# Kernel tuning notes

Measured on AMD Instinct MI355X. Metric: run time of the kernel, lower is better.

## Reference

```python
import jax, jax.numpy as jnp
import numpy as np

L_SEQ = 4096   # sequence length L
E = 1024       # embedding_size
NL = 8         # num_layers
H = 4 * E      # channel-mix hidden
V = 4          # LocalHilDim
LOGP_FACTOR = 0.5


def setup_inputs() -> dict:
    key = jax.random.key(0)
    ks = jax.random.split(key, 20)
    n = lambda k, shp, s=0.02: jax.random.normal(k, shp, jnp.float32) * s
    u = lambda k, shp: jax.random.uniform(k, shp, dtype=jnp.float32)
    return {
        "s": jax.random.randint(ks[0], (L_SEQ,), 0, V),
        "embed": n(ks[1], (V, E), 1.0),
        # TimeMixing params, stacked over layers
        "tm_first": jnp.log(jnp.float32(0.3)) + n(ks[2], (NL, E), 0.5),
        "tm_decay": -5.0 + 8.0 * u(ks[3], (NL, E)),
        "tm_mk": u(ks[4], (NL, E)),
        "tm_mv": u(ks[5], (NL, E)),
        "tm_mr": u(ks[6], (NL, E)),
        "tm_Wk": n(ks[7], (NL, E, E)),
        "tm_Wv": n(ks[8], (NL, E, E)),
        "tm_Wr": n(ks[9], (NL, E, E)),
        "tm_Wo": n(ks[10], (NL, E, E)),
        # ChannelMixing params
        "cm_mk": u(ks[11], (NL, E)),
        "cm_mr": u(ks[12], (NL, E)),
        "cm_Wk": n(ks[13], (NL, E, H)),
        "cm_Wr": n(ks[14], (NL, E, E)),
        "cm_Wv": n(ks[15], (NL, H, E)),
        # Neck / Head
        "neck_W": n(ks[16], (E, E)),
        "neck_b": jnp.zeros((E,), jnp.float32),
        "head_W": n(ks[17], (E, V)),
    }


def _wkv(k, v, time_first, time_decay):
    """Max-stabilized RWKV WKV recurrence over time. k,v: [L,E]."""
    z = jnp.zeros_like(k[0])
    init = (z, z, jnp.full_like(k[0], -jnp.inf))  # aa, bb, pp

    def step(carry, kv):
        aa, bb, pp = carry
        kk, vv = kv
        ww = time_first + kk
        p = jnp.maximum(pp, ww)
        e1 = jnp.exp(pp - p)
        e2 = jnp.exp(ww - p)
        out = (e1 * aa + e2 * vv) / (e1 * bb + e2)
        ww = pp - jnp.exp(time_decay)
        p = jnp.maximum(ww, kk)
        e1 = jnp.exp(ww - p)
        e2 = jnp.exp(kk - p)
        return (e1 * aa + e2 * vv, e1 * bb + e2, p), out

    _, out = jax.lax.scan(step, init, (k, v))
    return out


def _shift(x):
    # prepend zero-state row, drop last (token-shift with zero initial state)
    return jnp.concatenate([jnp.zeros_like(x[:1]), x[:-1]], axis=0)


def _block(x, p):
    # --- TimeMixing ---
    sx = _shift(x)
    kx = x * p["tm_mk"] + sx * (1 - p["tm_mk"])
    vx = x * p["tm_mv"] + sx * (1 - p["tm_mv"])
    rx = x * p["tm_mr"] + sx * (1 - p["tm_mr"])
    r = jax.nn.sigmoid(rx @ p["tm_Wr"])
    k = kx @ p["tm_Wk"]
    v = vx @ p["tm_Wv"]
    wkv = _wkv(k, v, p["tm_first"], p["tm_decay"])
    x = x + (r * wkv) @ p["tm_Wo"]
    # --- ChannelMixing ---
    sx = _shift(x)
    xk = x * p["cm_mk"] + sx * (1 - p["cm_mk"])
    xr = x * p["cm_mr"] + sx * (1 - p["cm_mr"])
    r = jax.nn.sigmoid(xr @ p["cm_Wr"])
    kk = jnp.square(jax.nn.relu(xk @ p["cm_Wk"]))  # [L, 4E]
    x = x + r * (kk @ p["cm_Wv"])
    return x


def reference(s, embed, tm_first, tm_decay, tm_mk, tm_mv, tm_mr,
              tm_Wk, tm_Wv, tm_Wr, tm_Wo, cm_mk, cm_mr, cm_Wk, cm_Wr, cm_Wv,
              neck_W, neck_b, head_W):
    tok = jnp.pad(s[:-1], (1, 0))
    x = embed[tok]                          # [L, E]
    layer_params = {
        "tm_first": tm_first, "tm_decay": tm_decay,
        "tm_mk": tm_mk, "tm_mv": tm_mv, "tm_mr": tm_mr,
        "tm_Wk": tm_Wk, "tm_Wv": tm_Wv, "tm_Wr": tm_Wr, "tm_Wo": tm_Wo,
        "cm_mk": cm_mk, "cm_mr": cm_mr,
        "cm_Wk": cm_Wk, "cm_Wr": cm_Wr, "cm_Wv": cm_Wv,
    }

    def body(x, p):
        return _block(x, p), None

    x, _ = jax.lax.scan(body, x, layer_params)  # scan over NL layers
    x = jax.nn.gelu(x @ neck_W + neck_b)
    logits = x @ head_W                         # [L, V]
    logp = jax.nn.log_softmax(logits) * LOGP_FACTOR
    # log-amplitude of configuration s (Q is None -> no mask, no penalty)
    return jnp.take_along_axis(logp, s[:, None], axis=-1).sum(axis=-2).squeeze(-1)
```

## Files before the change

### kernel.cpp

```cpp
#include <hip/hip_runtime.h>
#include <stdint.h>

#define L_SEQ 4096
#define EDIM  1024
#define HDIM  4096
#define NLAY  8
#define WKV_C 128
#define WKV_T 32
#define SCAN_LANES 16
#define SCAN_CPT   (WKV_C / SCAN_LANES)

typedef unsigned short u16;
typedef __attribute__((ext_vector_type(8))) short short8;
typedef __attribute__((ext_vector_type(4))) float f32x4;
typedef __attribute__((ext_vector_type(4))) unsigned short us4;
typedef __attribute__((ext_vector_type(8))) unsigned short us8;

static __device__ __forceinline__ u16 f2b(float f) {
  union { float f; uint32_t u; } a; a.f = f;
  uint32_t u = a.u;
  return (u16)((u + 0x7FFFu + ((u >> 16) & 1u)) >> 16);
}
static __device__ __forceinline__ float b2f(u16 b) {
  union { uint32_t u; float f; } a; a.u = ((uint32_t)b) << 16;
  return a.f;
}
static __device__ __forceinline__ float sigm(float v) {
  return 1.f / (1.f + __expf(-v));
}
static __device__ __forceinline__ float4 ld_bf4(const u16* __restrict__ p, size_t i) {
  us4 v = *reinterpret_cast<const us4*>(&p[i]);
  return make_float4(b2f(v.x), b2f(v.y), b2f(v.z), b2f(v.w));
}

static __device__ __forceinline__ void gld_lds16(const void* g, void* l) {
  __builtin_amdgcn_global_load_lds(
      (const __attribute__((address_space(1))) void*)g,
      (__attribute__((address_space(3))) void*)l, 16, 0, 0);
}


__global__ void k_f0(const int* __restrict__ s, const float* __restrict__ embed,
                     const float* __restrict__ mk, const float* __restrict__ mv,
                     const float* __restrict__ mr, u16* __restrict__ xA,
                     u16* __restrict__ kx, u16* __restrict__ vx, u16* __restrict__ rx) {
  int i = (blockIdx.x * blockDim.x + threadIdx.x) * 4;
  int t = i >> 10, e = i & 1023;
  int tok = (t == 0) ? 0 : s[t - 1];
  float4 xc = *reinterpret_cast<const float4*>(&embed[tok * EDIM + e]);
  float4 xs = make_float4(0.f, 0.f, 0.f, 0.f);
  if (t > 0) {
    int tokp = (t == 1) ? 0 : s[t - 2];
    xs = *reinterpret_cast<const float4*>(&embed[tokp * EDIM + e]);
  }
  us4 ox; ox.x = f2b(xc.x); ox.y = f2b(xc.y); ox.z = f2b(xc.z); ox.w = f2b(xc.w);
  *reinterpret_cast<us4*>(&xA[i]) = ox;
  float4 m; us4 o;
  m = *reinterpret_cast<const float4*>(&mk[e]);
  o.x = f2b(xc.x * m.x + xs.x * (1.f - m.x)); o.y = f2b(xc.y * m.y + xs.y * (1.f - m.y));
  o.z = f2b(xc.z * m.z + xs.z * (1.f - m.z)); o.w = f2b(xc.w * m.w + xs.w * (1.f - m.w));
  *reinterpret_cast<us4*>(&kx[i]) = o;
  m = *reinterpret_cast<const float4*>(&mv[e]);
  o.x = f2b(xc.x * m.x + xs.x * (1.f - m.x)); o.y = f2b(xc.y * m.y + xs.y * (1.f - m.y));
  o.z = f2b(xc.z * m.z + xs.z * (1.f - m.z)); o.w = f2b(xc.w * m.w + xs.w * (1.f - m.w));
  *reinterpret_cast<us4*>(&vx[i]) = o;
  m = *reinterpret_cast<const float4*>(&mr[e]);
  o.x = f2b(xc.x * m.x + xs.x * (1.f - m.x)); o.y = f2b(xc.y * m.y + xs.y * (1.f - m.y));
  o.z = f2b(xc.z * m.z + xs.z * (1.f - m.z)); o.w = f2b(xc.w * m.w + xs.w * (1.f - m.w));
  *reinterpret_cast<us4*>(&rx[i]) = o;
}

static __device__ __forceinline__ float4 cm_finish(const u16* __restrict__ xB,
                                                   const u16* __restrict__ PR,
                                                   const u16* __restrict__ PB, int i) {
  const size_t LE = (size_t)L_SEQ * EDIM;
  float4 xm = ld_bf4(xB, i);
  float4 r0 = ld_bf4(PR, i), r1 = ld_bf4(PR, i + LE);
  float4 v0 = ld_bf4(PB, i), v1 = ld_bf4(PB, i + LE);
  float4 v2 = ld_bf4(PB, i + 2 * LE), v3 = ld_bf4(PB, i + 3 * LE);
  xm.x += sigm(r0.x + r1.x) * (v0.x + v1.x + v2.x + v3.x);
  xm.y += sigm(r0.y + r1.y) * (v0.y + v1.y + v2.y + v3.y);
  xm.z += sigm(r0.z + r1.z) * (v0.z + v1.z + v2.z + v3.z);
  xm.w += sigm(r0.w + r1.w) * (v0.w + v1.w + v2.w + v3.w);
  return xm;
}

__global__ void k_f1(const u16* __restrict__ xB, const u16* __restrict__ PR,
                     const u16* __restrict__ PB,
                     const float* __restrict__ mk, const float* __restrict__ mv,
                     const float* __restrict__ mr, u16* __restrict__ xA,
                     u16* __restrict__ kx, u16* __restrict__ vx, u16* __restrict__ rx) {
  int i = (blockIdx.x * blockDim.x + threadIdx.x) * 4;
  int e = i & 1023;
  float4 xc = cm_finish(xB, PR, PB, i);
  float4 xs = make_float4(0.f, 0.f, 0.f, 0.f);
  if (i >= EDIM) xs = cm_finish(xB, PR, PB, i - EDIM);
  us4 ox; ox.x = f2b(xc.x); ox.y = f2b(xc.y); ox.z = f2b(xc.z); ox.w = f2b(xc.w);
  *reinterpret_cast<us4*>(&xA[i]) = ox;
  float4 m; us4 o;
  m = *reinterpret_cast<const float4*>(&mk[e]);
  o.x = f2b(xc.x * m.x + xs.x * (1.f - m.x)); o.y = f2b(xc.y * m.y + xs.y * (1.f - m.y));
  o.z = f2b(xc.z * m.z + xs.z * (1.f - m.z)); o.w = f2b(xc.w * m.w + xs.w * (1.f - m.w));
  *reinterpret_cast<us4*>(&kx[i]) = o;
  m = *reinterpret_cast<const float4*>(&mv[e]);
  o.x = f2b(xc.x * m.x + xs.x * (1.f - m.x)); o.y = f2b(xc.y * m.y + xs.y * (1.f - m.y));
  o.z = f2b(xc.z * m.z + xs.z * (1.f - m.z)); o.w = f2b(xc.w * m.w + xs.w * (1.f - m.w));
  *reinterpret_cast<us4*>(&vx[i]) = o;
  m = *reinterpret_cast<const float4*>(&mr[e]);
  o.x = f2b(xc.x * m.x + xs.x * (1.f - m.x)); o.y = f2b(xc.y * m.y + xs.y * (1.f - m.y));
  o.z = f2b(xc.z * m.z + xs.z * (1.f - m.z)); o.w = f2b(xc.w * m.w + xs.w * (1.f - m.w));
  *reinterpret_cast<us4*>(&rx[i]) = o;
}

static __device__ __forceinline__ float4 tm_finish(const u16* __restrict__ xA,
                                                   const u16* __restrict__ PA, int i) {
  const size_t LE = (size_t)L_SEQ * EDIM;
  float4 xm = ld_bf4(xA, i);
  float4 a = ld_bf4(PA, i), b = ld_bf4(PA, i + LE);
  xm.x += a.x + b.x; xm.y += a.y + b.y; xm.z += a.z + b.z; xm.w += a.w + b.w;
  return xm;
}

__global__ void k_f2(const u16* __restrict__ xA, const u16* __restrict__ PA,
                     const float* __restrict__ mk, const float* __restrict__ mr,
                     u16* __restrict__ xB, u16* __restrict__ kx, u16* __restrict__ rx) {
  int i = (blockIdx.x * blockDim.x + threadIdx.x) * 4;
  int e = i & 1023;
  float4 xc = tm_finish(xA, PA, i);
  float4 xs = make_float4(0.f, 0.f, 0.f, 0.f);
  if (i >= EDIM) xs = tm_finish(xA, PA, i - EDIM);
  us4 ox; ox.x = f2b(xc.x); ox.y = f2b(xc.y); ox.z = f2b(xc.z); ox.w = f2b(xc.w);
  *reinterpret_cast<us4*>(&xB[i]) = ox;
  float4 m; us4 o;
  m = *reinterpret_cast<const float4*>(&mk[e]);
  o.x = f2b(xc.x * m.x + xs.x * (1.f - m.x)); o.y = f2b(xc.y * m.y + xs.y * (1.f - m.y));
  o.z = f2b(xc.z * m.z + xs.z * (1.f - m.z)); o.w = f2b(xc.w * m.w + xs.w * (1.f - m.w));
  *reinterpret_cast<us4*>(&kx[i]) = o;
  m = *reinterpret_cast<const float4*>(&mr[e]);
  o.x = f2b(xc.x * m.x + xs.x * (1.f - m.x)); o.y = f2b(xc.y * m.y + xs.y * (1.f - m.y));
  o.z = f2b(xc.z * m.z + xs.z * (1.f - m.z)); o.w = f2b(xc.w * m.w + xs.w * (1.f - m.w));
  *reinterpret_cast<us4*>(&rx[i]) = o;
}

__global__ void k_f3(const u16* __restrict__ xB, const u16* __restrict__ PR,
                     const u16* __restrict__ PB, u16* __restrict__ hb) {
  int i = (blockIdx.x * blockDim.x + threadIdx.x) * 4;
  float4 xc = cm_finish(xB, PR, PB, i);
  us4 o;
  o.x = f2b(xc.x); o.y = f2b(xc.y); o.z = f2b(xc.z); o.w = f2b(xc.w);
  *reinterpret_cast<us4*>(&hb[i]) = o;
}

static __device__ __forceinline__ float gelu1(float v) {
  float c = 0.7978845608028654f * (v + 0.044715f * v * v * v);
  return 0.5f * v * (1.f + tanhf(c));
}

static __device__ __forceinline__
void tconv2(const float* __restrict__ s, u16* __restrict__ d, int K, int N,
            int n0, int k0) {
  __shared__ float tile[64][65];
  int tid = threadIdx.x;
  int tx = tid & 15, ty = tid >> 4;
#pragma unroll
  for (int i = 0; i < 4; ++i) {
    int kr = ty + i * 16;
    float4 v = *reinterpret_cast<const float4*>(&s[(size_t)(k0 + kr) * N + n0 + tx * 4]);
    tile[kr][tx * 4 + 0] = v.x; tile[kr][tx * 4 + 1] = v.y;
    tile[kr][tx * 4 + 2] = v.z; tile[kr][tx * 4 + 3] = v.w;
  }
  __syncthreads();
  int tx8 = tid & 7, ny = tid >> 3;
#pragma unroll
  for (int h = 0; h < 2; ++h) {
    int n = ny + h * 32;
    us8 o;
#pragma unroll
    for (int c = 0; c < 8; ++c) o[c] = f2b(tile[tx8 * 8 + c][n]);
    *reinterpret_cast<us8*>(&d[(size_t)(n0 + n) * K + k0 + tx8 * 8]) = o;
  }
}

__global__ __launch_bounds__(256)
void k_tconv(const float* __restrict__ src, u16* __restrict__ dst, int K, int N) {
  tconv2(src + (size_t)blockIdx.z * K * N, dst + (size_t)blockIdx.z * K * N,
         K, N, blockIdx.x * 64, blockIdx.y * 64);
}

#define TC_EE  (41 * 256)
#define TC_EH  8192
__global__ __launch_bounds__(256)
void k_tconv_all(const float* __restrict__ Wk, const float* __restrict__ Wv,
                 const float* __restrict__ Wr, const float* __restrict__ Wo,
                 const float* __restrict__ cWr, const float* __restrict__ nW,
                 const float* __restrict__ cWk, const float* __restrict__ cWv,
                 u16* __restrict__ oWk, u16* __restrict__ oWv, u16* __restrict__ oWr,
                 u16* __restrict__ oWo, u16* __restrict__ ocWr, u16* __restrict__ onW,
                 u16* __restrict__ ocWk, u16* __restrict__ ocWv) {
  const size_t EE = (size_t)EDIM * EDIM, EH = (size_t)EDIM * HDIM;
  int bid = blockIdx.x;
  if (bid < TC_EE) {
    int z = bid >> 8, rem = bid & 255;
    const float* src; u16* dst;
    if (z < 8)       { src = Wk  + (size_t)z * EE;        dst = oWk  + (size_t)z * EE; }
    else if (z < 16) { src = Wv  + (size_t)(z - 8) * EE;  dst = oWv  + (size_t)(z - 8) * EE; }
    else if (z < 24) { src = Wr  + (size_t)(z - 16) * EE; dst = oWr  + (size_t)(z - 16) * EE; }
    else if (z < 32) { src = Wo  + (size_t)(z - 24) * EE; dst = oWo  + (size_t)(z - 24) * EE; }
    else if (z < 40) { src = cWr + (size_t)(z - 32) * EE; dst = ocWr + (size_t)(z - 32) * EE; }
    else             { src = nW;                          dst = onW; }
    tconv2(src, dst, EDIM, EDIM, (rem & 15) * 64, (rem >> 4) * 64);
  } else if (bid < TC_EE + TC_EH) {
    int b = bid - TC_EE;
    int z = b >> 10, rem = b & 1023;
    tconv2(cWk + (size_t)z * EH, ocWk + (size_t)z * EH, EDIM, HDIM,
           (rem & 63) * 64, (rem >> 6) * 64);
  } else {
    int b = bid - TC_EE - TC_EH;
    int z = b >> 10, rem = b & 1023;
    tconv2(cWv + (size_t)z * EH, ocWv + (size_t)z * EH, HDIM, EDIM,
           (rem & 15) * 64, (rem >> 4) * 64);
  }
}

template <int EPI>
__device__ __forceinline__
void g256_body(const u16* __restrict__ A, const u16* __restrict__ Bt,
               void* __restrict__ Cv, int N, int ldk, int klen,
               int bm, int bn) {
  extern __shared__ __align__(16) u16 lds[];
  const int tid = threadIdx.x, lane = tid & 63, w = tid >> 6;
  const int wr = w >> 2, wc = w & 3;
  const int l16 = lane & 15, lhi = lane >> 4;
  const int NT = klen >> 5;

  f32x4 acc[8][4];
#pragma unroll
  for (int i = 0; i < 8; ++i)
#pragma unroll
    for (int j = 0; j < 4; ++j)
#pragma unroll
      for (int r = 0; r < 4; ++r) acc[i][j][r] = 0.f;

  const int sd = tid * 16;
  const int sr = sd >> 6;
  const int sc = ((sd >> 4) & 3) ^ ((sr >> 1) & 3);
  const int sdst = w * 512;

  const int spn = lhi ^ ((l16 >> 1) & 3);
  const int aBase = wr * 4096 + l16 * 32 + spn * 8;
  const int bBase = 8192 + (wc >> 1) * 4096 + ((wc & 1) * 64 + l16) * 32 + spn * 8;

  auto stage_ht = [&](int kt, int ht) {
    const u16* src = (ht < 2) ? A : Bt;
    int rowbase = ((ht < 2) ? bm : bn) + (ht & 1) * 128;
    gld_lds16(src + (size_t)(rowbase + sr) * ldk + kt * 32 + sc * 8,
              &lds[(kt & 3) * 16384 + ht * 4096 + sdst]);
  };

#pragma unroll
  for (int t = 0; t < 3; ++t)
#pragma unroll
    for (int h = 0; h < 4; ++h) stage_ht(t, h);
  asm volatile("s_waitcnt vmcnt(8)" ::: "memory");
  __builtin_amdgcn_s_barrier();

  short8 a[4], b[4];
  for (int kt = 0; kt < NT; ++kt) {
    const int pb = (kt & 3) * 16384;
    __builtin_amdgcn_sched_barrier(0);
#pragma unroll
    for (int mi = 0; mi < 4; ++mi)
      a[mi] = *reinterpret_cast<const short8*>(&lds[pb + aBase + mi * 512]);
#pragma unroll
    for (int ni = 0; ni < 4; ++ni)
      b[ni] = *reinterpret_cast<const short8*>(&lds[pb + bBase + ni * 512]);
    if (kt + 3 < NT) { stage_ht(kt + 3, 0); stage_ht(kt + 3, 1); }
    __builtin_amdgcn_s_barrier();
    asm volatile("s_waitcnt lgkmcnt(0)" ::: "memory");
    __builtin_amdgcn_sched_barrier(0);
    __builtin_amdgcn_s_setprio(1);
#pragma unroll
    for (int mi = 0; mi < 4; ++mi)
#pragma unroll
      for (int ni = 0; ni < 4; ++ni)
        acc[mi][ni] = __builtin_amdgcn_mfma_f32_16x16x32_bf16(a[mi], b[ni], acc[mi][ni], 0, 0, 0);
    __builtin_amdgcn_s_setprio(0);
    __builtin_amdgcn_s_barrier();
    __builtin_amdgcn_sched_barrier(0);
#pragma unroll
    for (int mi = 0; mi < 4; ++mi)
      a[mi] = *reinterpret_cast<const short8*>(&lds[pb + aBase + 2048 + mi * 512]);
    if (kt + 3 < NT) { stage_ht(kt + 3, 2); stage_ht(kt + 3, 3); }
    __builtin_amdgcn_s_barrier();
    asm volatile("s_waitcnt lgkmcnt(0)" ::: "memory");
    __builtin_amdgcn_sched_barrier(0);
    __builtin_amdgcn_s_setprio(1);
#pragma unroll
    for (int mi = 0; mi < 4; ++mi)
#pragma unroll
      for (int ni = 0; ni < 4; ++ni)
        acc[4 + mi][ni] = __builtin_amdgcn_mfma_f32_16x16x32_bf16(a[mi], b[ni], acc[4 + mi][ni], 0, 0, 0);
    __builtin_amdgcn_s_setprio(0);
    if (kt + 4 <= NT)      asm volatile("s_waitcnt vmcnt(8)" ::: "memory");
    else if (kt + 3 == NT) asm volatile("s_waitcnt vmcnt(4)" ::: "memory");
    else if (kt + 2 == NT) asm volatile("s_waitcnt vmcnt(0)" ::: "memory");
    __builtin_amdgcn_s_barrier();
  }

#pragma unroll
  for (int q = 0; q < 8; ++q)
#pragma unroll
    for (int ni = 0; ni < 4; ++ni)
#pragma unroll
      for (int r = 0; r < 4; ++r) {
        int row = bm + wr * 128 + (q >> 2) * 64 + (q & 3) * 16 + lhi * 4 + r;
        int col = bn + wc * 64 + ni * 16 + l16;
        size_t o = (size_t)row * N + col;
        float v = acc[q][ni][r];
        if constexpr (EPI == 0) ((float*)Cv)[o] = v;
        else if constexpr (EPI == 1) ((u16*)Cv)[o] = f2b(v);
        else { v = fmaxf(v, 0.f); ((u16*)Cv)[o] = f2b(v * v); }
      }
}

__global__ __launch_bounds__(512)
void k_g256_cmk(const u16* __restrict__ A, const u16* __restrict__ Bt,
                u16* __restrict__ C) {
  int bid = blockIdx.x;
  int wg = (bid & 7) * 32 + (bid >> 3);
  int lb = wg & 3, sv = wg >> 2;
  int by = (sv >> 3) * 2 + (lb & 1);
  int bx = (sv & 7) * 2 + (lb >> 1);
  g256_body<2>(A, Bt, C, HDIM, EDIM, EDIM, by * 256, bx * 256);
}

__global__ __launch_bounds__(512)
void k_g256_wv(const u16* __restrict__ A, const u16* __restrict__ Bt,
               u16* __restrict__ P) {
  int bid = blockIdx.x;
  int wg = (bid & 7) * 32 + (bid >> 3);
  int z = wg >> 6, rem = wg & 63;
  int lb = rem & 3, sv = rem >> 2;
  int by = (sv >> 1) * 2 + (lb & 1);
  int bx = (sv & 1) * 2 + (lb >> 1);
  g256_body<1>(A + z * 1024, Bt + z * 1024, P + (size_t)z * L_SEQ * EDIM,
               EDIM, HDIM, 1024, by * 256, bx * 256);
}

__global__ __launch_bounds__(512)
void k_g256_3(const u16* __restrict__ A0, const u16* __restrict__ A1, const u16* __restrict__ A2,
              const u16* __restrict__ B0, const u16* __restrict__ B1, const u16* __restrict__ B2,
              u16* __restrict__ C0, u16* __restrict__ C1, u16* __restrict__ C2) {
  int bid = blockIdx.x;
  int wg = (bid & 7) * 24 + (bid >> 3);
  int z = wg >> 6, rem = wg & 63;
  int lb = rem & 3, sv = rem >> 2;
  int by = (sv >> 1) * 2 + (lb & 1);
  int bx = (sv & 1) * 2 + (lb >> 1);
  const u16* A = (z == 0) ? A0 : (z == 1) ? A1 : A2;
  const u16* B = (z == 0) ? B0 : (z == 1) ? B1 : B2;
  u16*       C = (z == 0) ? C0 : (z == 1) ? C1 : C2;
  g256_body<1>(A, B, C, EDIM, EDIM, EDIM, by * 256, bx * 256);
}

__device__ __forceinline__
void g128_body(const u16* __restrict__ A, const u16* __restrict__ Bt,
               u16* __restrict__ Cv, int N, int ldk, int klen,
               int bm, int bn) {
  extern __shared__ __align__(16) u16 lds[];
  const int tid = threadIdx.x, lane = tid & 63, w = tid >> 6;
  const int wr = w >> 2, wc = w & 3;
  const int l16 = lane & 15, lhi = lane >> 4;
  const int NT = klen >> 5;

  f32x4 acc[8][2];
#pragma unroll
  for (int i = 0; i < 8; ++i)
#pragma unroll
    for (int j = 0; j < 2; ++j)
#pragma unroll
      for (int r = 0; r < 4; ++r) acc[i][j][r] = 0.f;

  const int sd = tid * 16;
  const int sr = sd >> 6;
  const int sc = ((sd >> 4) & 3) ^ ((sr >> 1) & 3);
  const int sdst = w * 512;

  const int spn = lhi ^ ((l16 >> 1) & 3);
  const int aBase = wr * 4096 + l16 * 32 + spn * 8;
  const int bBase = 8192 + (wc * 32 + l16) * 32 + spn * 8;

  auto stage_ht = [&](int kt, int ht) {
    const u16* src = (ht < 2) ? A : Bt;
    int rowbase = (ht < 2) ? (bm + ht * 128) : bn;
    int dsto = (ht < 2) ? ht * 4096 : 8192;
    gld_lds16(src + (size_t)(rowbase + sr) * ldk + kt * 32 + sc * 8,
              &lds[(kt & 3) * 12288 + dsto + sdst]);
  };

#pragma unroll
  for (int t = 0; t < 3; ++t) {
    stage_ht(t, 0); stage_ht(t, 1); stage_ht(t, 2);
  }
  asm volatile("s_waitcnt vmcnt(6)" ::: "memory");
  __builtin_amdgcn_s_barrier();

  short8 a[4], b[2];
  for (int kt = 0; kt < NT; ++kt) {
    const int pb = (kt & 3) * 12288;
    __builtin_amdgcn_sched_barrier(0);
#pragma unroll
    for (int mi = 0; mi < 4; ++mi)
      a[mi] = *reinterpret_cast<const short8*>(&lds[pb + aBase + mi * 512]);
#pragma unroll
    for (int ni = 0; ni < 2; ++ni)
      b[ni] = *reinterpret_cast<const short8*>(&lds[pb + bBase + ni * 512]);
    if (kt + 3 < NT) { stage_ht(kt + 3, 0); stage_ht(kt + 3, 1); }
    __builtin_amdgcn_s_barrier();
    asm volatile("s_waitcnt lgkmcnt(0)" ::: "memory");
    __builtin_amdgcn_sched_barrier(0);
    __builtin_amdgcn_s_setprio(1);
#pragma unroll
    for (int mi = 0; mi < 4; ++mi)
#pragma unroll
      for (int ni = 0; ni < 2; ++ni)
        acc[mi][ni] = __builtin_amdgcn_mfma_f32_16x16x32_bf16(a[mi], b[ni], acc[mi][ni], 0, 0, 0);
    __builtin_amdgcn_s_setprio(0);
    __builtin_amdgcn_s_barrier();
    __builtin_amdgcn_sched_barrier(0);
#pragma unroll
    for (int mi = 0; mi < 4; ++mi)
      a[mi] = *reinterpret_cast<const short8*>(&lds[pb + aBase + 2048 + mi * 512]);
    if (kt + 3 < NT) stage_ht(kt + 3, 2);
    __builtin_amdgcn_s_barrier();
    asm volatile("s_waitcnt lgkmcnt(0)" ::: "memory");
    __builtin_amdgcn_sched_barrier(0);
    __builtin_amdgcn_s_setprio(1);
#pragma unroll
    for (int mi = 0; mi < 4; ++mi)
#pragma unroll
      for (int ni = 0; ni < 2; ++ni)
        acc[4 + mi][ni] = __builtin_amdgcn_mfma_f32_16x16x32_bf16(a[mi], b[ni], acc[4 + mi][ni], 0, 0, 0);
    __builtin_amdgcn_s_setprio(0);
    if (kt + 4 <= NT)      asm volatile("s_waitcnt vmcnt(6)" ::: "memory");
    else if (kt + 3 == NT) asm volatile("s_waitcnt vmcnt(3)" ::: "memory");
    else if (kt + 2 == NT) asm volatile("s_waitcnt vmcnt(0)" ::: "memory");
    __builtin_amdgcn_s_barrier();
  }

#pragma unroll
  for (int q = 0; q < 8; ++q)
#pragma unroll
    for (int ni = 0; ni < 2; ++ni)
#pragma unroll
      for (int r = 0; r < 4; ++r) {
        int row = bm + wr * 128 + (q >> 2) * 64 + (q & 3) * 16 + lhi * 4 + r;
        int col = bn + wc * 32 + ni * 16 + l16;
        Cv[(size_t)row * N + col] = f2b(acc[q][ni][r]);
      }
}

__global__ __launch_bounds__(512)
void k_gx128_sk2(const u16* __restrict__ A, const u16* __restrict__ Bt,
                 u16* __restrict__ P) {
  int bid = blockIdx.x;
  int wg = (bid & 7) * 32 + (bid >> 3);
  int z = wg >> 7, rem = wg & 127;
  int by = rem >> 3, bx = rem & 7;
  g128_body(A + z * 512, Bt + z * 512, P + (size_t)z * L_SEQ * EDIM,
            EDIM, EDIM, 512, by * 256, bx * 128);
}


__global__ void k_wkv_pass1(const u16* __restrict__ k, const u16* __restrict__ v,
                            const float* __restrict__ w_,
                            float* __restrict__ sa, float* __restrict__ sb,
                            float* __restrict__ sp) {
  int id = blockIdx.x * blockDim.x + threadIdx.x;
  int e = id & 1023, c = id >> 10;
  float D = __expf(w_[e]);
  float aa = 0.f, bb = 0.f, pp = -__builtin_inff();
  const u16* kp = k + (size_t)c * WKV_T * EDIM + e;
  const u16* vp = v + (size_t)c * WKV_T * EDIM + e;
#pragma unroll 4
  for (int i = 0; i < WKV_T; ++i) {
    float kk = b2f(kp[i * EDIM]), vv = b2f(vp[i * EDIM]);
    float ww = pp - D;
    float p2 = fmaxf(ww, kk);
    float e1 = __expf(ww - p2), e2 = __expf(kk - p2);
    aa = e1 * aa + e2 * vv;
    bb = e1 * bb + e2;
    pp = p2;
  }
  sa[id] = aa; sb[id] = bb; sp[id] = pp;
}

__global__ __launch_bounds__(256)
void k_wkv_scan16(const float* __restrict__ w_,
                  const float* __restrict__ sa, const float* __restrict__ sb,
                  const float* __restrict__ sp,
                  float* __restrict__ oa, float* __restrict__ ob,
                  float* __restrict__ op) {
  int t = blockIdx.x * blockDim.x + threadIdx.x;
  int e = t >> 4, j = t & (SCAN_LANES - 1);
  const float NEG = -1e30f;
  float DT = __expf(w_[e]) * (float)WKV_T;
  float Ea[SCAN_CPT], Eb[SCAN_CPT], Ep[SCAN_CPT];
  float A = 0.f, B = 0.f, P = NEG;
  int base = j * SCAN_CPT;
#pragma unroll
  for (int i = 0; i < SCAN_CPT; ++i) {
    int idx = (base + i) * EDIM + e;
    Ea[i] = A; Eb[i] = B; Ep[i] = P;
    float a = sa[idx], b = sb[idx], q = sp[idx];
    float shift = P - DT;
    float pn = fmaxf(shift, q);
    float w1 = __expf(shift - pn), w2 = __expf(q - pn);
    A = w1 * A + w2 * a; B = w1 * B + w2 * b; P = pn;
  }
  float tA = A, tB = B, tP = P; int tn = SCAN_CPT;
#pragma unroll
  for (int d = 1; d < SCAN_LANES; d <<= 1) {
    float fA = __shfl_up(tA, d, SCAN_LANES);
    float fB = __shfl_up(tB, d, SCAN_LANES);
    float fP = __shfl_up(tP, d, SCAN_LANES);
    int   fn = __shfl_up(tn, d, SCAN_LANES);
    if (j >= d) {
      float shift = fP - DT * (float)tn;
      float pn = fmaxf(shift, tP);
      float w1 = __expf(shift - pn), w2 = __expf(tP - pn);
      tA = w1 * fA + w2 * tA; tB = w1 * fB + w2 * tB; tP = pn; tn += fn;
    }
  }
  float pA = __shfl_up(tA, 1, SCAN_LANES);
  float pB = __shfl_up(tB, 1, SCAN_LANES);
  float pP = __shfl_up(tP, 1, SCAN_LANES);
  if (j == 0) { pA = 0.f; pB = 0.f; pP = NEG; }
#pragma unroll
  for (int i = 0; i < SCAN_CPT; ++i) {
    float shift = pP - DT * (float)i;
    float pn = fmaxf(shift, Ep[i]);
    float w1 = __expf(shift - pn), w2 = __expf(Ep[i] - pn);
    int idx = (base + i) * EDIM + e;
    oa[idx] = w1 * pA + w2 * Ea[i];
    ob[idx] = w1 * pB + w2 * Eb[i];
    op[idx] = pn;
  }
}

__global__ void k_wkv_pass2(const u16* __restrict__ k, const u16* __restrict__ v,
                            const float* __restrict__ u_, const float* __restrict__ w_,
                            const float* __restrict__ sa, const float* __restrict__ sb,
                            const float* __restrict__ sp,
                            const u16* __restrict__ rpre, u16* __restrict__ rwb) {
  int id = blockIdx.x * blockDim.x + threadIdx.x;
  int e = id & 1023, c = id >> 10;
  float u = u_[e];
  float D = __expf(w_[e]);
  float aa = sa[id], bb = sb[id], pp = sp[id];
  const size_t base = (size_t)c * WKV_T * EDIM + e;
  const u16* kp = k + base;
  const u16* vp = v + base;
  const u16* rp = rpre + base;
  u16* op = rwb + base;
#pragma unroll 4
  for (int i = 0; i < WKV_T; ++i) {
    float kk = b2f(kp[i * EDIM]), vv = b2f(vp[i * EDIM]);
    float ww = u + kk;
    float p = fmaxf(pp, ww);
    float e1 = __expf(pp - p), e2 = __expf(ww - p);
    float out = (e1 * aa + e2 * vv) / (e1 * bb + e2);
    op[i * EDIM] = f2b(out * sigm(b2f(rp[i * EDIM])));
    float w2s = pp - D;
    float p2 = fmaxf(w2s, kk);
    float e1b = __expf(w2s - p2), e2b = __expf(kk - p2);
    aa = e1b * aa + e2b * vv;
    bb = e1b * bb + e2b;
    pp = p2;
  }
}

__global__ __launch_bounds__(256)
void k_head(const u16* __restrict__ P, const float* __restrict__ nb,
            const float* __restrict__ W,
            const int* __restrict__ s, float* __restrict__ partial) {
  const size_t LE = (size_t)L_SEQ * EDIM;
  int t = blockIdx.x, tid = threadIdx.x;
  float a0 = 0.f, a1 = 0.f, a2 = 0.f, a3 = 0.f;
  for (int e = tid; e < EDIM; e += 256) {
    size_t i = (size_t)t * EDIM + e;
    float hv = gelu1(b2f(P[i]) + b2f(P[i + LE]) + nb[e]);
    const float4 wv = *reinterpret_cast<const float4*>(W + e * 4);
    a0 += hv * wv.x; a1 += hv * wv.y; a2 += hv * wv.z; a3 += hv * wv.w;
  }
#pragma unroll
  for (int off = 32; off > 0; off >>= 1) {
    a0 += __shfl_down(a0, off, 64);
    a1 += __shfl_down(a1, off, 64);
    a2 += __shfl_down(a2, off, 64);
    a3 += __shfl_down(a3, off, 64);
  }
  __shared__ float sm[4][4];
  int w = tid >> 6, lane = tid & 63;
  if (lane == 0) { sm[w][0] = a0; sm[w][1] = a1; sm[w][2] = a2; sm[w][3] = a3; }
  __syncthreads();
  if (tid == 0) {
    float lg[4];
#pragma unroll
    for (int j = 0; j < 4; ++j) lg[j] = sm[0][j] + sm[1][j] + sm[2][j] + sm[3][j];
    float m = fmaxf(fmaxf(lg[0], lg[1]), fmaxf(lg[2], lg[3]));
    float sum = expf(lg[0] - m) + expf(lg[1] - m) + expf(lg[2] - m) + expf(lg[3] - m);
    partial[t] = 0.5f * (lg[s[t]] - m - logf(sum));
  }
}

__global__ __launch_bounds__(256)
void k_reduce(const float* __restrict__ partial, float* __restrict__ out) {
  int tid = threadIdx.x;
  float a = 0.f;
  for (int j = tid; j < L_SEQ; j += 256) a += partial[j];
#pragma unroll
  for (int off = 32; off > 0; off >>= 1) a += __shfl_down(a, off, 64);
  __shared__ float sm[4];
  if ((tid & 63) == 0) sm[tid >> 6] = a;
  __syncthreads();
  if (tid == 0) out[0] = sm[0] + sm[1] + sm[2] + sm[3];
}


extern "C" void kernel_launch(void* const* d_in, const int* in_sizes, int n_in,
                              void* d_out, int out_size, void* d_ws, size_t ws_size,
                              hipStream_t stream) {
  const int*   s        = (const int*)d_in[0];
  const float* embed    = (const float*)d_in[1];
  const float* tm_first = (const float*)d_in[2];
  const float* tm_decay = (const float*)d_in[3];
  const float* tm_mk    = (const float*)d_in[4];
  const float* tm_mv    = (const float*)d_in[5];
  const float* tm_mr    = (const float*)d_in[6];
  const float* tm_Wk    = (const float*)d_in[7];
  const float* tm_Wv    = (const float*)d_in[8];
  const float* tm_Wr    = (const float*)d_in[9];
  const float* tm_Wo    = (const float*)d_in[10];
  const float* cm_mk    = (const float*)d_in[11];
  const float* cm_mr    = (const float*)d_in[12];
  const float* cm_Wk    = (const float*)d_in[13];
  const float* cm_Wr    = (const float*)d_in[14];
  const float* cm_Wv    = (const float*)d_in[15];
  const float* neck_W   = (const float*)d_in[16];
  const float* neck_b   = (const float*)d_in[17];
  const float* head_W   = (const float*)d_in[18];

  char* ws = (char*)d_ws;
  size_t off = 0;
  auto alloc = [&](size_t bytes) { char* p = ws + off; off += (bytes + 255) & ~(size_t)255; return p; };
  const size_t LE2 = (size_t)L_SEQ * EDIM * 2;
  const size_t EE  = (size_t)EDIM * EDIM, EH = (size_t)EDIM * HDIM;

  u16*   xA    = (u16*)alloc(LE2);
  u16*   xB    = (u16*)alloc(LE2);
  u16*   kxb   = (u16*)alloc(LE2);
  u16*   vxb   = (u16*)alloc(LE2);
  u16*   rxb   = (u16*)alloc(LE2);
  u16*   kf    = (u16*)alloc(LE2);
  u16*   vf    = (u16*)alloc(LE2);
  u16*   rpre  = (u16*)alloc(LE2);
  u16*   kkb   = (u16*)alloc((size_t)L_SEQ * HDIM * 2);
  u16*   PA    = (u16*)alloc(2 * LE2);
  u16*   PR    = (u16*)alloc(2 * LE2);
  u16*   PB    = (u16*)alloc(4 * LE2);
  float* partial = (float*)alloc((size_t)L_SEQ * 4);
  float* sa  = (float*)alloc((size_t)WKV_C * EDIM * 4);
  float* sb  = (float*)alloc((size_t)WKV_C * EDIM * 4);
  float* sp  = (float*)alloc((size_t)WKV_C * EDIM * 4);
  float* sa2 = (float*)alloc((size_t)WKV_C * EDIM * 4);
  float* sb2 = (float*)alloc((size_t)WKV_C * EDIM * 4);
  float* sp2 = (float*)alloc((size_t)WKV_C * EDIM * 4);

  size_t remain = (ws_size > off) ? ws_size - off : 0;
  const size_t bigNeed = (5 * EE * NLAY + 2 * EH * NLAY + EE) * 2 + 16 * 256;
  const bool big = remain >= bigNeed;
  const int NB = big ? NLAY : 1;
  u16* wWk   = (u16*)alloc(EE * NB * 2);
  u16* wWv   = (u16*)alloc(EE * NB * 2);
  u16* wWr   = (u16*)alloc(EE * NB * 2);
  u16* wWo   = (u16*)alloc(EE * NB * 2);
  u16* wcmWr = (u16*)alloc(EE * NB * 2);
  u16* wcmWk = (u16*)alloc(EH * NB * 2);
  u16* wcmWv = (u16*)alloc(EH * NB * 2);
  u16* wneck = big ? (u16*)alloc(EE * 2) : wWk;

  const dim3 blk(256);
  const dim3 blk512(512);
  const dim3 gE4((L_SEQ * EDIM) / 1024);
  const dim3 gWkv((WKV_C * EDIM) / 256);
  const dim3 gScan((EDIM * SCAN_LANES) / 256);
  const size_t DLDS  = 131072;
  const size_t DLDS2 = 98304;

  if (big) {
    k_tconv_all<<<dim3(TC_EE + 2 * TC_EH), blk, 0, stream>>>(
        tm_Wk, tm_Wv, tm_Wr, tm_Wo, cm_Wr, neck_W, cm_Wk, cm_Wv,
        wWk, wWv, wWr, wWo, wcmWr, wneck, wcmWk, wcmWv);
  }

  for (int l = 0; l < NLAY; ++l) {
    size_t oE  = (size_t)l * EDIM;
    size_t oEE = (size_t)l * EE;
    size_t oEH = (size_t)l * EH;
    size_t wE  = big ? oEE : 0;
    size_t wH  = big ? oEH : 0;
    if (!big) {
      k_tconv<<<dim3(EDIM / 64, EDIM / 64, 1), blk, 0, stream>>>(tm_Wk + oEE, wWk, EDIM, EDIM);
      k_tconv<<<dim3(EDIM / 64, EDIM / 64, 1), blk, 0, stream>>>(tm_Wv + oEE, wWv, EDIM, EDIM);
      k_tconv<<<dim3(EDIM / 64, EDIM / 64, 1), blk, 0, stream>>>(tm_Wr + oEE, wWr, EDIM, EDIM);
      k_tconv<<<dim3(EDIM / 64, EDIM / 64, 1), blk, 0, stream>>>(tm_Wo + oEE, wWo, EDIM, EDIM);
      k_tconv<<<dim3(EDIM / 64, EDIM / 64, 1), blk, 0, stream>>>(cm_Wr + oEE, wcmWr, EDIM, EDIM);
      k_tconv<<<dim3(HDIM / 64, EDIM / 64, 1), blk, 0, stream>>>(cm_Wk + oEH, wcmWk, EDIM, HDIM);
      k_tconv<<<dim3(EDIM / 64, HDIM / 64, 1), blk, 0, stream>>>(cm_Wv + oEH, wcmWv, HDIM, EDIM);
    }
    if (l == 0)
      k_f0<<<gE4, blk, 0, stream>>>(s, embed, tm_mk + oE, tm_mv + oE, tm_mr + oE,
                                    xA, kxb, vxb, rxb);
    else
      k_f1<<<gE4, blk, 0, stream>>>(xB, PR, PB, tm_mk + oE, tm_mv + oE, tm_mr + oE,
                                    xA, kxb, vxb, rxb);
    k_g256_3<<<dim3(192), blk512, DLDS, stream>>>(kxb, vxb, rxb,
                                                  wWk + wE, wWv + wE, wWr + wE,
                                                  kf, vf, rpre);
    k_wkv_pass1<<<gWkv, blk, 0, stream>>>(kf, vf, tm_decay + oE, sa, sb, sp);
    k_wkv_scan16<<<gScan, blk, 0, stream>>>(tm_decay + oE, sa, sb, sp, sa2, sb2, sp2);
    k_wkv_pass2<<<gWkv, blk, 0, stream>>>(kf, vf, tm_first + oE, tm_decay + oE,
                                          sa2, sb2, sp2, rpre, vxb);
    k_gx128_sk2<<<dim3(256), blk512, DLDS2, stream>>>(vxb, wWo + wE, PA);
    k_f2<<<gE4, blk, 0, stream>>>(xA, PA, cm_mk + oE, cm_mr + oE, xB, kxb, rxb);
    k_gx128_sk2<<<dim3(256), blk512, DLDS2, stream>>>(rxb, wcmWr + wE, PR);
    k_g256_cmk<<<dim3(256), blk512, DLDS, stream>>>(kxb, wcmWk + wH, kkb);
    k_g256_wv<<<dim3(256), blk512, DLDS, stream>>>(kkb, wcmWv + wH, PB);
  }
  if (!big) k_tconv<<<dim3(EDIM / 64, EDIM / 64, 1), blk, 0, stream>>>(neck_W, wneck, EDIM, EDIM);
  k_f3<<<gE4, blk, 0, stream>>>(xB, PR, PB, kxb);
  k_gx128_sk2<<<dim3(256), blk512, DLDS2, stream>>>(kxb, wneck, PA);
  k_head<<<dim3(L_SEQ), blk, 0, stream>>>(PA, neck_b, head_W, s, partial);
  k_reduce<<<dim3(1), blk, 0, stream>>>(partial, (float*)d_out);

  (void)in_sizes; (void)n_in; (void)out_size;
}
```

Before: 1.778 ms.

## Fuse channel-mix Wr and Wk GEMMs into one launch; retile QKV GEMM

The channel-mix receptance GEMM (split-K 128-wide tiles) and the channel-mix key GEMM (256x256 tiles with squared-ReLU epilogue) now run in a single 512-block launch, with the block index choosing which body to run. This removes one launch and lets the smaller GEMM fill the machine alongside the larger one. The three time-mix K/V/R projections switch from 192 blocks of 256x256 tiles to 384 blocks of 256x128 tiles to raise occupancy across CUs. Weight-transpose loads also become nontemporal. Smaller tiles cost more operand reloads, and the fused kernel has to reserve the larger LDS allocation for every block.

```diff
diff --git a/kernel.cpp b/kernel.cpp
--- a/kernel.cpp
+++ b/kernel.cpp
@@ -13,6 +13,7 @@
 typedef unsigned short u16;
 typedef __attribute__((ext_vector_type(8))) short short8;
 typedef __attribute__((ext_vector_type(4))) float f32x4;
+typedef __attribute__((ext_vector_type(4))) float f4v;
 typedef __attribute__((ext_vector_type(4))) unsigned short us4;
 typedef __attribute__((ext_vector_type(8))) unsigned short us8;
 
@@ -165,7 +166,8 @@
 #pragma unroll
   for (int i = 0; i < 4; ++i) {
     int kr = ty + i * 16;
-    float4 v = *reinterpret_cast<const float4*>(&s[(size_t)(k0 + kr) * N + n0 + tx * 4]);
+    f4v v = __builtin_nontemporal_load(
+        reinterpret_cast<const f4v*>(&s[(size_t)(k0 + kr) * N + n0 + tx * 4]));
     tile[kr][tx * 4 + 0] = v.x; tile[kr][tx * 4 + 1] = v.y;
     tile[kr][tx * 4 + 2] = v.z; tile[kr][tx * 4 + 3] = v.w;
   }
@@ -323,16 +325,103 @@
       }
 }
 
-__global__ __launch_bounds__(512)
-void k_g256_cmk(const u16* __restrict__ A, const u16* __restrict__ Bt,
-                u16* __restrict__ C) {
-  int bid = blockIdx.x;
-  int wg = (bid & 7) * 32 + (bid >> 3);
-  int lb = wg & 3, sv = wg >> 2;
-  int by = (sv >> 3) * 2 + (lb & 1);
-  int bx = (sv & 7) * 2 + (lb >> 1);
-  g256_body<2>(A, Bt, C, HDIM, EDIM, EDIM, by * 256, bx * 256);
-}
+__device__ __forceinline__
+void g128_body(const u16* __restrict__ A, const u16* __restrict__ Bt,
+               u16* __restrict__ Cv, int N, int ldk, int klen,
+               int bm, int bn) {
+  extern __shared__ __align__(16) u16 lds[];
+  const int tid = threadIdx.x, lane = tid & 63, w = tid >> 6;
+  const int wr = w >> 2, wc = w & 3;
+  const int l16 = lane & 15, lhi = lane >> 4;
+  const int NT = klen >> 5;
+
+  f32x4 acc[8][2];
+#pragma unroll
+  for (int i = 0; i < 8; ++i)
+#pragma unroll
+    for (int j = 0; j < 2; ++j)
+#pragma unroll
+      for (int r = 0; r < 4; ++r) acc[i][j][r] = 0.f;
+
+  const int sd = tid * 16;
+  const int sr = sd >> 6;
+  const int sc = ((sd >> 4) & 3) ^ ((sr >> 1) & 3);
+  const int sdst = w * 512;
+
+  const int spn = lhi ^ ((l16 >> 1) & 3);
+  const int aBase = wr * 4096 + l16 * 32 + spn * 8;
+  const int bBase = 8192 + (wc * 32 + l16) * 32 + spn * 8;
+
+  auto stage_ht = [&](int kt, int ht) {
+    const u16* src = (ht < 2) ? A : Bt;
+    int rowbase = (ht < 2) ? (bm + ht * 128) : bn;
+    int dsto = (ht < 2) ? ht * 4096 : 8192;
+    gld_lds16(src + (size_t)(rowbase + sr) * ldk + kt * 32 + sc * 8,
+              &lds[(kt & 3) * 12288 + dsto + sdst]);
+  };
+
+#pragma unroll
+  for (int t = 0; t < 3; ++t) {
+    stage_ht(t, 0); stage_ht(t, 1); stage_ht(t, 2);
+  }
+  asm volatile("s_waitcnt vmcnt(6)" ::: "memory");
+  __builtin_amdgcn_s_barrier();
+
+  short8 a[4], b[2];
+  for (int kt = 0; kt < NT; ++kt) {
+    const int pb = (kt & 3) * 12288;
+    __builtin_amdgcn_sched_barrier(0);
+#pragma unroll
+    for (int mi = 0; mi < 4; ++mi)
+      a[mi] = *reinterpret_cast<const short8*>(&lds[pb + aBase + mi * 512]);
+#pragma unroll
+    for (int ni = 0; ni < 2; ++ni)
+      b[ni] = *reinterpret_cast<const short8*>(&lds[pb + bBase + ni * 512]);
+    if (kt + 3 < NT) { stage_ht(kt + 3, 0); stage_ht(kt + 3, 1); }
+    __builtin_amdgcn_s_barrier();
+    asm volatile("s_waitcnt lgkmcnt(0)" ::: "memory");
+    __builtin_amdgcn_sched_barrier(0);
+    __builtin_amdgcn_s_setprio(1);
+#pragma unroll
+    for (int mi = 0; mi < 4; ++mi)
+#pragma unroll
+      for (int ni = 0; ni < 2; ++ni)
+        acc[mi][ni] = __builtin_amdgcn_mfma_f32_16x16x32_bf16(a[mi], b[ni], acc[mi][ni], 0, 0, 0);
+    __builtin_amdgcn_s_setprio(0);
+    __builtin_amdgcn_s_barrier();
+    __builtin_amdgcn_sched_barrier(0);
+#pragma unroll
+    for (int mi = 0; mi < 4; ++mi)
+      a[mi] = *reinterpret_cast<const short8*>(&lds[pb + aBase + 2048 + mi * 512]);
+    if (kt + 3 < NT) stage_ht(kt + 3, 2);
+    __builtin_amdgcn_s_barrier();
+    asm volatile("s_waitcnt lgkmcnt(0)" ::: "memory");
+    __builtin_amdgcn_sched_barrier(0);
+    __builtin_amdgcn_s_setprio(1);
+#pragma unroll
+    for (int mi = 0; mi < 4; ++mi)
+#pragma unroll
+      for (int ni = 0; ni < 2; ++ni)
+        acc[4 + mi][ni] = __builtin_amdgcn_mfma_f32_16x16x32_bf16(a[mi], b[ni], acc[4 + mi][ni], 0, 0, 0);
+    __builtin_amdgcn_s_setprio(0);
+    if (kt + 4 <= NT)      asm volatile("s_waitcnt vmcnt(6)" ::: "memory");
+    else if (kt + 3 == NT) asm volatile("s_waitcnt vmcnt(3)" ::: "memory");
+    else if (kt + 2 == NT) asm volatile("s_waitcnt vmcnt(0)" ::: "memory");
+    __builtin_amdgcn_s_barrier();
+  }
+
+#pragma unroll
+  for (int q = 0; q < 8; ++q)
+#pragma unroll
+    for (int ni = 0; ni < 2; ++ni)
+#pragma unroll
+      for (int r = 0; r < 4; ++r) {
+        int row = bm + wr * 128 + (q >> 2) * 64 + (q & 3) * 16 + lhi * 4 + r;
+        int col = bn + wc * 32 + ni * 16 + l16;
+        Cv[(size_t)row * N + col] = f2b(acc[q][ni][r]);
+      }
+}
+
 
 __global__ __launch_bounds__(512)
 void k_g256_wv(const u16* __restrict__ A, const u16* __restrict__ Bt,
@@ -348,116 +437,39 @@
 }
 
 __global__ __launch_bounds__(512)
-void k_g256_3(const u16* __restrict__ A0, const u16* __restrict__ A1, const u16* __restrict__ A2,
+void k_g256_cm(const u16* __restrict__ kxb, const u16* __restrict__ Wk,
+               u16* __restrict__ kkb,
+               const u16* __restrict__ rxb, const u16* __restrict__ Wr,
+               u16* __restrict__ PR) {
+  int bid = blockIdx.x;
+  if (bid < 256) {
+    int wg = (bid & 7) * 32 + (bid >> 3);
+    int lb = wg & 3, sv = wg >> 2;
+    int by = (sv >> 3) * 2 + (lb & 1);
+    int bx = (sv & 7) * 2 + (lb >> 1);
+    g256_body<2>(kxb, Wk, kkb, HDIM, EDIM, EDIM, by * 256, bx * 256);
+  } else {
+    int b = bid - 256;
+    int wg = (b & 7) * 32 + (b >> 3);
+    int z = wg >> 7, rem = wg & 127;
+    int by = rem >> 3, bx = rem & 7;
+    g128_body(rxb + z * 512, Wr + z * 512, PR + (size_t)z * L_SEQ * EDIM,
+              EDIM, EDIM, 512, by * 256, bx * 128);
+  }
+}
+
+__global__ __launch_bounds__(512)
+void k_g128_3(const u16* __restrict__ A0, const u16* __restrict__ A1, const u16* __restrict__ A2,
               const u16* __restrict__ B0, const u16* __restrict__ B1, const u16* __restrict__ B2,
               u16* __restrict__ C0, u16* __restrict__ C1, u16* __restrict__ C2) {
   int bid = blockIdx.x;
-  int wg = (bid & 7) * 24 + (bid >> 3);
-  int z = wg >> 6, rem = wg & 63;
-  int lb = rem & 3, sv = rem >> 2;
-  int by = (sv >> 1) * 2 + (lb & 1);
-  int bx = (sv & 1) * 2 + (lb >> 1);
+  int wg = (bid & 7) * 48 + (bid >> 3);
+  int z = wg >> 7, rem = wg & 127;
+  int by = rem >> 3, bx = rem & 7;
   const u16* A = (z == 0) ? A0 : (z == 1) ? A1 : A2;
   const u16* B = (z == 0) ? B0 : (z == 1) ? B1 : B2;
   u16*       C = (z == 0) ? C0 : (z == 1) ? C1 : C2;
-  g256_body<1>(A, B, C, EDIM, EDIM, EDIM, by * 256, bx * 256);
-}
-
-__device__ __forceinline__
-void g128_body(const u16* __restrict__ A, const u16* __restrict__ Bt,
-               u16* __restrict__ Cv, int N, int ldk, int klen,
-               int bm, int bn) {
-  extern __shared__ __align__(16) u16 lds[];
-  const int tid = threadIdx.x, lane = tid & 63, w = tid >> 6;
-  const int wr = w >> 2, wc = w & 3;
-  const int l16 = lane & 15, lhi = lane >> 4;
-  const int NT = klen >> 5;
-
-  f32x4 acc[8][2];
-#pragma unroll
-  for (int i = 0; i < 8; ++i)
-#pragma unroll
-    for (int j = 0; j < 2; ++j)
-#pragma unroll
-      for (int r = 0; r < 4; ++r) acc[i][j][r] = 0.f;
-
-  const int sd = tid * 16;
-  const int sr = sd >> 6;
-  const int sc = ((sd >> 4) & 3) ^ ((sr >> 1) & 3);
-  const int sdst = w * 512;
-
-  const int spn = lhi ^ ((l16 >> 1) & 3);
-  const int aBase = wr * 4096 + l16 * 32 + spn * 8;
-  const int bBase = 8192 + (wc * 32 + l16) * 32 + spn * 8;
-
-  auto stage_ht = [&](int kt, int ht) {
-    const u16* src = (ht < 2) ? A : Bt;
-    int rowbase = (ht < 2) ? (bm + ht * 128) : bn;
-    int dsto = (ht < 2) ? ht * 4096 : 8192;
-    gld_lds16(src + (size_t)(rowbase + sr) * ldk + kt * 32 + sc * 8,
-              &lds[(kt & 3) * 12288 + dsto + sdst]);
-  };
-
-#pragma unroll
-  for (int t = 0; t < 3; ++t) {
-    stage_ht(t, 0); stage_ht(t, 1); stage_ht(t, 2);
-  }
-  asm volatile("s_waitcnt vmcnt(6)" ::: "memory");
-  __builtin_amdgcn_s_barrier();
-
-  short8 a[4], b[2];
-  for (int kt = 0; kt < NT; ++kt) {
-    const int pb = (kt & 3) * 12288;
-    __builtin_amdgcn_sched_barrier(0);
-#pragma unroll
-    for (int mi = 0; mi < 4; ++mi)
-      a[mi] = *reinterpret_cast<const short8*>(&lds[pb + aBase + mi * 512]);
-#pragma unroll
-    for (int ni = 0; ni < 2; ++ni)
-      b[ni] = *reinterpret_cast<const short8*>(&lds[pb + bBase + ni * 512]);
-    if (kt + 3 < NT) { stage_ht(kt + 3, 0); stage_ht(kt + 3, 1); }
-    __builtin_amdgcn_s_barrier();
-    asm volatile("s_waitcnt lgkmcnt(0)" ::: "memory");
-    __builtin_amdgcn_sched_barrier(0);
-    __builtin_amdgcn_s_setprio(1);
-#pragma unroll
-    for (int mi = 0; mi < 4; ++mi)
-#pragma unroll
-      for (int ni = 0; ni < 2; ++ni)
-        acc[mi][ni] = __builtin_amdgcn_mfma_f32_16x16x32_bf16(a[mi], b[ni], acc[mi][ni], 0, 0, 0);
-    __builtin_amdgcn_s_setprio(0);
-    __builtin_amdgcn_s_barrier();
-    __builtin_amdgcn_sched_barrier(0);
-#pragma unroll
-    for (int mi = 0; mi < 4; ++mi)
-      a[mi] = *reinterpret_cast<const short8*>(&lds[pb + aBase + 2048 + mi * 512]);
-    if (kt + 3 < NT) stage_ht(kt + 3, 2);
-    __builtin_amdgcn_s_barrier();
-    asm volatile("s_waitcnt lgkmcnt(0)" ::: "memory");
-    __builtin_amdgcn_sched_barrier(0);
-    __builtin_amdgcn_s_setprio(1);
-#pragma unroll
-    for (int mi = 0; mi < 4; ++mi)
-#pragma unroll
-      for (int ni = 0; ni < 2; ++ni)
-        acc[4 + mi][ni] = __builtin_amdgcn_mfma_f32_16x16x32_bf16(a[mi], b[ni], acc[4 + mi][ni], 0, 0, 0);
-    __builtin_amdgcn_s_setprio(0);
-    if (kt + 4 <= NT)      asm volatile("s_waitcnt vmcnt(6)" ::: "memory");
-    else if (kt + 3 == NT) asm volatile("s_waitcnt vmcnt(3)" ::: "memory");
-    else if (kt + 2 == NT) asm volatile("s_waitcnt vmcnt(0)" ::: "memory");
-    __builtin_amdgcn_s_barrier();
-  }
-
-#pragma unroll
-  for (int q = 0; q < 8; ++q)
-#pragma unroll
-    for (int ni = 0; ni < 2; ++ni)
-#pragma unroll
-      for (int r = 0; r < 4; ++r) {
-        int row = bm + wr * 128 + (q >> 2) * 64 + (q & 3) * 16 + lhi * 4 + r;
-        int col = bn + wc * 32 + ni * 16 + l16;
-        Cv[(size_t)row * N + col] = f2b(acc[q][ni][r]);
-      }
+  g128_body(A, B, C, EDIM, EDIM, EDIM, by * 256, bx * 128);
 }
 
 __global__ __launch_bounds__(512)
@@ -725,17 +737,17 @@
     else
       k_f1<<<gE4, blk, 0, stream>>>(xB, PR, PB, tm_mk + oE, tm_mv + oE, tm_mr + oE,
                                     xA, kxb, vxb, rxb);
-    k_g256_3<<<dim3(192), blk512, DLDS, stream>>>(kxb, vxb, rxb,
-                                                  wWk + wE, wWv + wE, wWr + wE,
-                                                  kf, vf, rpre);
+    k_g128_3<<<dim3(384), blk512, DLDS2, stream>>>(kxb, vxb, rxb,
+                                                   wWk + wE, wWv + wE, wWr + wE,
+                                                   kf, vf, rpre);
     k_wkv_pass1<<<gWkv, blk, 0, stream>>>(kf, vf, tm_decay + oE, sa, sb, sp);
     k_wkv_scan16<<<gScan, blk, 0, stream>>>(tm_decay + oE, sa, sb, sp, sa2, sb2, sp2);
     k_wkv_pass2<<<gWkv, blk, 0, stream>>>(kf, vf, tm_first + oE, tm_decay + oE,
                                           sa2, sb2, sp2, rpre, vxb);
     k_gx128_sk2<<<dim3(256), blk512, DLDS2, stream>>>(vxb, wWo + wE, PA);
     k_f2<<<gE4, blk, 0, stream>>>(xA, PA, cm_mk + oE, cm_mr + oE, xB, kxb, rxb);
-    k_gx128_sk2<<<dim3(256), blk512, DLDS2, stream>>>(rxb, wcmWr + wE, PR);
-    k_g256_cmk<<<dim3(256), blk512, DLDS, stream>>>(kxb, wcmWk + wH, kkb);
+    k_g256_cm<<<dim3(512), blk512, DLDS, stream>>>(kxb, wcmWk + wH, kkb,
+                                                   rxb, wcmWr + wE, PR);
     k_g256_wv<<<dim3(256), blk512, DLDS, stream>>>(kkb, wcmWv + wH, PB);
   }
   if (!big) k_tconv<<<dim3(EDIM / 64, EDIM / 64, 1), blk, 0, stream>>>(neck_W, wneck, EDIM, EDIM);
```

After: 1.816 ms. +2.1%, slower.
